# Kernel tuning notes

Measured on AMD Instinct MI355X. Metric: run time of the kernel, lower is better.

The kernel has to match this reference:

```python
import jax, jax.numpy as jnp
import numpy as np

B, F = 65536, 300
SIGMA = 2.0
ALPHA = 1.0


def _gaussian_kernel(sigma):
    l = int(np.round(3 * sigma + 1.0))  # 7 for sigma=2
    x = np.linspace(-(l - 1.0) / 2.0, (l - 1.0) / 2.0, l)
    k = np.exp(-0.5 * np.square(x) / np.square(sigma))
    return (k / k.sum()).astype(np.float32)


def setup_inputs() -> dict:
    key = jax.random.key(0)
    fr_funcs = jax.random.normal(key, (B, F), dtype=jnp.float32)
    freqs = np.arange(1, F + 1, dtype=np.float32)
    freqs = (freqs - freqs.min()) / (freqs.max() - freqs.min())
    freqs = freqs * 2.0 - 1.0  # normalized to [-1, 1], as in __init__
    return {
        "fr_funcs": fr_funcs,
        "freqs": jnp.asarray(freqs),
        "kernel": jnp.asarray(_gaussian_kernel(SIGMA)),
    }


def _first_peak_loss(f, freqs):
    # Replicates softlocalmax's first segment.
    # find_peaks on symmetric-padded signal => boundary is a peak iff it
    # strictly exceeds its single neighbor; interior peaks are strict local maxima.
    n = f.shape[0]
    interior = (f[1:-1] > f[:-2]) & (f[1:-1] > f[2:])
    is_peak = jnp.concatenate([f[0:1] > f[1:2], interior, f[-1:] > f[-2:-1]])
    idx = jnp.where(is_peak, jnp.arange(n, dtype=jnp.int32), n)
    two = jnp.sort(idx)[:2]  # first two peak positions (n if absent)
    npeaks = jnp.sum(is_peak.astype(jnp.int32))
    # first segment end: midpoint of first two peaks (int truncation), else n-1
    end = jnp.where(npeaks >= 2, (two[0] + two[1]) // 2, n - 1)
    mask = jnp.arange(n) < end
    logits = jnp.where(mask, f * ALPHA, -jnp.inf)
    w = jax.nn.softmax(logits)  # zeros outside segment == softmax over slice
    softargmax = w @ freqs
    return -softargmax


def reference(fr_funcs, freqs, kernel):
    # Gaussian1DBlur: conv1d with padding='same' (zero padding, odd kernel)
    blurred = jax.lax.conv_general_dilated(
        fr_funcs[:, None, :], kernel[None, None, :], (1,), "SAME"
    )[:, 0]  # (B, F)
    return jax.vmap(_first_peak_loss, in_axes=(0, None))(blurred, freqs)
```

## Files before the change

kernel.cpp:

```cpp
#include <hip/hip_runtime.h>
#include <math.h>

#define NF 300
#define NC 75

#define CONV(b0,b1,b2,b3,c0,c1,c2,A,B) \
    b0 = kk[0]*c0;  b0=fmaf(kk[1],c1 ,b0); b0=fmaf(kk[2],c2 ,b0); b0=fmaf(kk[3],A.x,b0); b0=fmaf(kk[4],A.y,b0); b0=fmaf(kk[5],A.z,b0); b0=fmaf(kk[6],A.w,b0); \
    b1 = kk[0]*c1;  b1=fmaf(kk[1],c2 ,b1); b1=fmaf(kk[2],A.x,b1); b1=fmaf(kk[3],A.y,b1); b1=fmaf(kk[4],A.z,b1); b1=fmaf(kk[5],A.w,b1); b1=fmaf(kk[6],B.x,b1); \
    b2 = kk[0]*c2;  b2=fmaf(kk[1],A.x,b2); b2=fmaf(kk[2],A.y,b2); b2=fmaf(kk[3],A.z,b2); b2=fmaf(kk[4],A.w,b2); b2=fmaf(kk[5],B.x,b2); b2=fmaf(kk[6],B.y,b2); \
    b3 = kk[0]*A.x; b3=fmaf(kk[1],A.y,b3); b3=fmaf(kk[2],A.z,b3); b3=fmaf(kk[3],A.w,b3); b3=fmaf(kk[4],B.x,b3); b3=fmaf(kk[5],B.y,b3); b3=fmaf(kk[6],B.z,b3);

#define PKCHK(J,V) { if (cnt==0) p0=(J); else if (cnt==1) p1=(J); ++cnt; (void)(V); }

__global__ __launch_bounds__(256) void peak_mover_loss_kernel(
    const float* __restrict__ in,
    const float* __restrict__ freqs,
    const float* __restrict__ kw,
    float* __restrict__ out)
{
    const int row = blockIdx.x * blockDim.x + threadIdx.x;
    const float4* rp4 = reinterpret_cast<const float4*>(in + (size_t)row * NF);

    float kk[7];
#pragma unroll
    for (int t = 0; t < 7; ++t) kk[t] = kw[t];

    float4 ch[8];
#pragma unroll
    for (int t = 0; t < 8; ++t) ch[t] = rp4[t];

    float bl[28];
    float c0 = 0.f, c1 = 0.f, c2 = 0.f;
    float prev1 = -INFINITY, prev2 = -INFINITY;
    int cnt = 0, p0 = 0, p1 = 0;
#pragma unroll
    for (int m = 0; m < 7; ++m) {
        float b0, b1, b2, b3;
        CONV(b0, b1, b2, b3, c0, c1, c2, ch[m], ch[m + 1]);
        bl[4*m] = b0; bl[4*m+1] = b1; bl[4*m+2] = b2; bl[4*m+3] = b3;
        const int base = 4 * m;
        if (prev1 > prev2 && prev1 > b0) PKCHK(base - 1, 0)
        if (b0 > prev1 && b0 > b1)       PKCHK(base,     0)
        if (b1 > b0 && b1 > b2)          PKCHK(base + 1, 0)
        if (b2 > b1 && b2 > b3)          PKCHK(base + 2, 0)
        prev2 = b2; prev1 = b3;
        c0 = ch[m].y; c1 = ch[m].z; c2 = ch[m].w;
    }
    float4 A4 = ch[7];

    int mc = 7;
#pragma unroll 1
    while (cnt < 2 && mc < NC) {
        float4 cc[17];
        cc[0] = A4;
#pragma unroll
        for (int t = 1; t <= 16; ++t) {
            const int idx = mc + t;
            float4 v = make_float4(0.f, 0.f, 0.f, 0.f);
            if (idx < NC) v = rp4[idx];
            cc[t] = v;
        }
#pragma unroll
        for (int t = 0; t < 16; ++t) {
            const int m = mc + t;
            if (m < NC && cnt < 2) {
                float b0, b1, b2, b3;
                CONV(b0, b1, b2, b3, c0, c1, c2, cc[t], cc[t + 1]);
                const int base = 4 * m;
                if (prev1 > prev2 && prev1 > b0) PKCHK(base - 1, 0)
                if (b0 > prev1 && b0 > b1)       PKCHK(base,     0)
                if (b1 > b0 && b1 > b2)          PKCHK(base + 1, 0)
                if (b2 > b1 && b2 > b3)          PKCHK(base + 2, 0)
                if (m == NC - 1 && cnt < 2 && b3 > b2) PKCHK(NF - 1, 0)
                prev2 = b2; prev1 = b3;
                c0 = cc[t].y; c1 = cc[t].z; c2 = cc[t].w;
            }
        }
        A4 = cc[16];
        mc += 16;
    }

    const int end = (cnt >= 2) ? ((p0 + p1) >> 1) : (NF - 1);

    const float fsc = 2.0f / 299.0f;
    float s = 0.f, tt = 0.f;
    if (end <= 28) {
#pragma unroll
        for (int j = 0; j < 28; ++j) {
            if (j < end) {
                const float e = __expf(bl[j]);
                s += e;
                tt = fmaf(e, fmaf((float)j, fsc, -1.f), tt);
            }
        }
    } else {
        float d0 = 0.f, d1 = 0.f, d2 = 0.f;
        float4 A = rp4[0], B = rp4[1], C = rp4[2], D = rp4[3];
        int m = 0;
#pragma unroll 1
        while (4 * m < end) {
            float b0, b1, b2, b3;
            CONV(b0, b1, b2, b3, d0, d1, d2, A, B);
            const int base = 4 * m;
            if (base     < end) { float e=__expf(b0); s+=e; tt=fmaf(e, fmaf((float)(base  ), fsc, -1.f), tt); }
            if (base + 1 < end) { float e=__expf(b1); s+=e; tt=fmaf(e, fmaf((float)(base+1), fsc, -1.f), tt); }
            if (base + 2 < end) { float e=__expf(b2); s+=e; tt=fmaf(e, fmaf((float)(base+2), fsc, -1.f), tt); }
            if (base + 3 < end) { float e=__expf(b3); s+=e; tt=fmaf(e, fmaf((float)(base+3), fsc, -1.f), tt); }
            d0 = A.y; d1 = A.z; d2 = A.w;
            A = B; B = C; C = D;
            const int k = m + 4;
            float4 nd = make_float4(0.f, 0.f, 0.f, 0.f);
            if (k < NC) nd = rp4[k];
            D = nd;
            ++m;
        }
    }

    out[row] = -(tt / s);
}

extern "C" void kernel_launch(void* const* d_in, const int* in_sizes, int n_in,
                              void* d_out, int out_size, void* d_ws, size_t ws_size,
                              hipStream_t stream) {
    const float* fr    = (const float*)d_in[0];
    const float* freqs = (const float*)d_in[1];
    const float* kw    = (const float*)d_in[2];
    float* outp = (float*)d_out;

    const int nrows = in_sizes[0] / NF;
    const int block = 256;
    const int grid  = nrows / block;
    peak_mover_loss_kernel<<<grid, block, 0, stream>>>(fr, freqs, kw, outp);
}
```

Measured before the change: 107.6 us.

## Widen prefetched row chunk and add wavefront-uniform early exits

Prefetches 14 float4s per row instead of 8, so the unrolled first pass covers 52 blurred values and fewer rows fall into the slow rescan path. Adds wave-wide __all/__any checks to stop the unrolled convolution once every lane has found two peaks, and to stop the softmax loop once no lane needs more terms. Sets launch_bounds minimum blocks to 1, letting the compiler use more registers for the larger arrays. The risk is lower occupancy and more bytes loaded per row for lanes that did not need them.

```diff
diff --git a/kernel.cpp b/kernel.cpp
--- a/kernel.cpp
+++ b/kernel.cpp
@@ -3,6 +3,8 @@
 
 #define NF 300
 #define NC 75
+#define CH 14
+#define BL (4*CH-4)
 
 #define CONV(b0,b1,b2,b3,c0,c1,c2,A,B) \
     b0 = kk[0]*c0;  b0=fmaf(kk[1],c1 ,b0); b0=fmaf(kk[2],c2 ,b0); b0=fmaf(kk[3],A.x,b0); b0=fmaf(kk[4],A.y,b0); b0=fmaf(kk[5],A.z,b0); b0=fmaf(kk[6],A.w,b0); \
@@ -10,9 +12,9 @@
     b2 = kk[0]*c2;  b2=fmaf(kk[1],A.x,b2); b2=fmaf(kk[2],A.y,b2); b2=fmaf(kk[3],A.z,b2); b2=fmaf(kk[4],A.w,b2); b2=fmaf(kk[5],B.x,b2); b2=fmaf(kk[6],B.y,b2); \
     b3 = kk[0]*A.x; b3=fmaf(kk[1],A.y,b3); b3=fmaf(kk[2],A.z,b3); b3=fmaf(kk[3],A.w,b3); b3=fmaf(kk[4],B.x,b3); b3=fmaf(kk[5],B.y,b3); b3=fmaf(kk[6],B.z,b3);
 
-#define PKCHK(J,V) { if (cnt==0) p0=(J); else if (cnt==1) p1=(J); ++cnt; (void)(V); }
+#define PKCHK(J) { if (cnt==0) p0=(J); else if (cnt==1) p1=(J); ++cnt; }
 
-__global__ __launch_bounds__(256) void peak_mover_loss_kernel(
+__global__ __launch_bounds__(256, 1) void peak_mover_loss_kernel(
     const float* __restrict__ in,
     const float* __restrict__ freqs,
     const float* __restrict__ kw,
@@ -20,35 +22,37 @@
 {
     const int row = blockIdx.x * blockDim.x + threadIdx.x;
     const float4* rp4 = reinterpret_cast<const float4*>(in + (size_t)row * NF);
+    (void)freqs;
+
+    float4 ch[CH];
+#pragma unroll
+    for (int t = 0; t < CH; ++t) ch[t] = rp4[t];
 
     float kk[7];
 #pragma unroll
     for (int t = 0; t < 7; ++t) kk[t] = kw[t];
 
-    float4 ch[8];
-#pragma unroll
-    for (int t = 0; t < 8; ++t) ch[t] = rp4[t];
-
-    float bl[28];
+    float bl[BL];
     float c0 = 0.f, c1 = 0.f, c2 = 0.f;
     float prev1 = -INFINITY, prev2 = -INFINITY;
     int cnt = 0, p0 = 0, p1 = 0;
 #pragma unroll
-    for (int m = 0; m < 7; ++m) {
+    for (int m = 0; m < CH - 1; ++m) {
+        if (m >= 2 && (m & 1) == 0) { if (__all(cnt >= 2)) break; }
         float b0, b1, b2, b3;
         CONV(b0, b1, b2, b3, c0, c1, c2, ch[m], ch[m + 1]);
         bl[4*m] = b0; bl[4*m+1] = b1; bl[4*m+2] = b2; bl[4*m+3] = b3;
         const int base = 4 * m;
-        if (prev1 > prev2 && prev1 > b0) PKCHK(base - 1, 0)
-        if (b0 > prev1 && b0 > b1)       PKCHK(base,     0)
-        if (b1 > b0 && b1 > b2)          PKCHK(base + 1, 0)
-        if (b2 > b1 && b2 > b3)          PKCHK(base + 2, 0)
+        if (prev1 > prev2 && prev1 > b0) PKCHK(base - 1)
+        if (b0 > prev1 && b0 > b1)       PKCHK(base)
+        if (b1 > b0 && b1 > b2)          PKCHK(base + 1)
+        if (b2 > b1 && b2 > b3)          PKCHK(base + 2)
         prev2 = b2; prev1 = b3;
         c0 = ch[m].y; c1 = ch[m].z; c2 = ch[m].w;
     }
-    float4 A4 = ch[7];
+    float4 A4 = ch[CH - 1];
 
-    int mc = 7;
+    int mc = CH - 1;
 #pragma unroll 1
     while (cnt < 2 && mc < NC) {
         float4 cc[17];
@@ -67,11 +71,11 @@
                 float b0, b1, b2, b3;
                 CONV(b0, b1, b2, b3, c0, c1, c2, cc[t], cc[t + 1]);
                 const int base = 4 * m;
-                if (prev1 > prev2 && prev1 > b0) PKCHK(base - 1, 0)
-                if (b0 > prev1 && b0 > b1)       PKCHK(base,     0)
-                if (b1 > b0 && b1 > b2)          PKCHK(base + 1, 0)
-                if (b2 > b1 && b2 > b3)          PKCHK(base + 2, 0)
-                if (m == NC - 1 && cnt < 2 && b3 > b2) PKCHK(NF - 1, 0)
+                if (prev1 > prev2 && prev1 > b0) PKCHK(base - 1)
+                if (b0 > prev1 && b0 > b1)       PKCHK(base)
+                if (b1 > b0 && b1 > b2)          PKCHK(base + 1)
+                if (b2 > b1 && b2 > b3)          PKCHK(base + 2)
+                if (m == NC - 1 && cnt < 2 && b3 > b2) PKCHK(NF - 1)
                 prev2 = b2; prev1 = b3;
                 c0 = cc[t].y; c1 = cc[t].z; c2 = cc[t].w;
             }
@@ -84,13 +88,18 @@
 
     const float fsc = 2.0f / 299.0f;
     float s = 0.f, tt = 0.f;
-    if (end <= 28) {
+    if (end <= BL) {
 #pragma unroll
-        for (int j = 0; j < 28; ++j) {
-            if (j < end) {
-                const float e = __expf(bl[j]);
-                s += e;
-                tt = fmaf(e, fmaf((float)j, fsc, -1.f), tt);
+        for (int jb = 0; jb < BL; jb += 4) {
+            if (!__any(jb < end)) break;
+#pragma unroll
+            for (int e = 0; e < 4; ++e) {
+                const int j = jb + e;
+                if (j < end) {
+                    const float ev = __expf(bl[j]);
+                    s += ev;
+                    tt = fmaf(ev, fmaf((float)j, fsc, -1.f), tt);
+                }
             }
         }
     } else {
```

Result: faster. 105.4 us (median of 2 runs) (-2.0%).
